# Kernel optimization log

Measured on AMD Instinct MI355X. Metric: run time of the kernel, lower is better.

Reference implementation:

```python
import jax, jax.numpy as jnp
import numpy as np

L, S, B, E, H, FF = 512, 2048, 4, 1024, 16, 2048
HD = E // H  # 64


def _layernorm(x, g, b, eps=1e-5):
    m = jnp.mean(x, axis=-1, keepdims=True)
    v = jnp.mean((x - m) ** 2, axis=-1, keepdims=True)
    return (x - m) * jax.lax.rsqrt(v + eps) * g + b


def _decoder(tgt, memory, pos, query_pos,
             in_proj_w, in_proj_b, out_w, out_b,
             cq_w, cq_b, ck_w, ck_b, cv_w, cv_b,
             down_w, down_b, lin1_w, lin1_b, lin2_w, lin2_b,
             n1_g, n1_b, n2_g, n2_b, n3_g, n3_b):
    Lq, Bb, Em = tgt.shape
    scale = 1.0 / np.sqrt(HD).astype(np.float32)
    # --- self attention (torch nn.MultiheadAttention, eval mode, no masks) ---
    qk_in = tgt + query_pos
    Wq, Wk, Wv = jnp.split(in_proj_w, 3, axis=0)
    bq, bk, bv = jnp.split(in_proj_b, 3)
    q = (qk_in @ Wq.T + bq).reshape(Lq, Bb, H, HD)
    k = (qk_in @ Wk.T + bk).reshape(Lq, Bb, H, HD)
    v = (tgt @ Wv.T + bv).reshape(Lq, Bb, H, HD)
    attn = jax.nn.softmax(jnp.einsum('lbhd,mbhd->bhlm', q, k) * scale, axis=-1)
    ctx = jnp.einsum('bhlm,mbhd->lbhd', attn, v).reshape(Lq, Bb, Em)
    tgt = _layernorm(tgt + ctx @ out_w.T + out_b, n1_g, n1_b)
    # --- custom cross attention; inputs permuted to [B, E, N] (Conv1d k=1 == matmul) ---
    qc = jnp.einsum('oe,lbe->bol', cq_w, tgt + query_pos) + cq_b[None, :, None]
    kc = jnp.einsum('oe,sbe->bos', ck_w, memory + pos) + ck_b[None, :, None]
    vc = jnp.einsum('oe,sbe->bos', cv_w, memory) + cv_b[None, :, None]
    # view(B, head_dim, num_heads, N): channel axis splits as (HD, H)
    qc = qc.reshape(Bb, HD, H, -1)
    kc = kc.reshape(Bb, HD, H, -1)
    vc = vc.reshape(Bb, HD, H, -1)
    # scores_2[b,d,h,m] = kc[b,d,h,m] * sum_{d',n} qc[b,d',h,n] kc[b,d',h,m] / sqrt(HD)
    # (einsum('abcd,aced->abcd', key, scores_1) broadcasts key over the summed n axis)
    s1sum = jnp.einsum('bdh,bdhm->bhm', qc.sum(-1), kc) * scale
    prob = jax.nn.softmax(kc * s1sum[:, None, :, :], axis=-1)        # [B,HD,H,S]
    o = jnp.einsum('bnhm,bdhm->bdhn', prob, vc)                       # [B,HD,H,HD]
    o = (o @ down_w.T + down_b).reshape(Bb, Em, 1)                    # Linear HD->1, then view
    tgt = _layernorm(tgt + jnp.transpose(o, (2, 0, 1)), n2_g, n2_b)   # [1,B,E] broadcasts over L
    # --- FFN ---
    ff = jax.nn.relu(tgt @ lin1_w.T + lin1_b) @ lin2_w.T + lin2_b
    return _layernorm(tgt + ff, n3_g, n3_b)


def setup_inputs() -> dict:
    key = jax.random.key(0)
    ks = jax.random.split(key, 16)
    def nrm(k, shape, s=0.02):
        return (s * jax.random.normal(k, shape)).astype(jnp.float32)
    z = lambda *s: jnp.zeros(s, jnp.float32)
    return dict(
        tgt=nrm(ks[0], (L, B, E), 1.0),
        memory=nrm(ks[1], (S, B, E), 1.0),
        pos=nrm(ks[2], (S, B, E), 1.0),
        query_pos=nrm(ks[3], (L, B, E), 1.0),
        in_proj_w=nrm(ks[4], (3 * E, E)), in_proj_b=z(3 * E),
        out_w=nrm(ks[5], (E, E)), out_b=z(E),
        cq_w=nrm(ks[6], (E, E)), cq_b=z(E),
        ck_w=nrm(ks[7], (E, E)), ck_b=z(E),
        cv_w=nrm(ks[8], (E, E)), cv_b=z(E),
        down_w=nrm(ks[9], (1, HD)), down_b=z(1),
        lin1_w=nrm(ks[10], (FF, E)), lin1_b=z(FF),
        lin2_w=nrm(ks[11], (E, FF)), lin2_b=z(E),
        n1_g=jnp.ones((E,), jnp.float32), n1_b=z(E),
        n2_g=jnp.ones((E,), jnp.float32), n2_b=z(E),
        n3_g=jnp.ones((E,), jnp.float32), n3_b=z(E),
    )


def reference(tgt, memory, pos, query_pos,
              in_proj_w, in_proj_b, out_w, out_b,
              cq_w, cq_b, ck_w, ck_b, cv_w, cv_b,
              down_w, down_b, lin1_w, lin1_b, lin2_w, lin2_b,
              n1_g, n1_b, n2_g, n2_b, n3_g, n3_b):
    return _decoder(tgt, memory, pos, query_pos,
                    in_proj_w, in_proj_b, out_w, out_b,
                    cq_w, cq_b, ck_w, ck_b, cv_w, cv_b,
                    down_w, down_b, lin1_w, lin1_b, lin2_w, lin2_b,
                    n1_g, n1_b, n2_g, n2_b, n3_g, n3_b)
```

## Files before the change

kernel.cpp:

```cpp
#include <hip/hip_runtime.h>
#include <hip/hip_bf16.h>

typedef __hip_bfloat16 bf16;
typedef short short8 __attribute__((ext_vector_type(8)));
typedef float f32x4 __attribute__((ext_vector_type(4)));

#define Lq 512
#define Sm 2048
#define Bb 4
#define Ee 1024
#define Hh 16
#define FFd 2048
#define HDd 64

static __device__ __forceinline__ float b2f(bf16 x) { return __bfloat162float(x); }
static __device__ __forceinline__ bf16 f2b(float x) { return __float2bfloat16(x); }
static __device__ __forceinline__ unsigned short bits(bf16 x) {
    return __builtin_bit_cast(unsigned short, x);
}
static __device__ __forceinline__ float us2f(unsigned short u) {
    return b2f(__builtin_bit_cast(bf16, u));
}

static __device__ __forceinline__ void gload16(const void* g, void* l) {
    __builtin_amdgcn_global_load_lds(
        (const __attribute__((address_space(1))) unsigned int*)g,
        (__attribute__((address_space(3))) unsigned int*)l, 16, 0, 0);
}

static __device__ __forceinline__ short8 pack8(float4 a0, float4 a1) {
    short8 u;
    u[0] = (short)bits(f2b(a0.x)); u[1] = (short)bits(f2b(a0.y));
    u[2] = (short)bits(f2b(a0.z)); u[3] = (short)bits(f2b(a0.w));
    u[4] = (short)bits(f2b(a1.x)); u[5] = (short)bits(f2b(a1.y));
    u[6] = (short)bits(f2b(a1.z)); u[7] = (short)bits(f2b(a1.w));
    return u;
}

__global__ __launch_bounds__(512, 2)
void kcvc_gemm(const bf16* __restrict__ wk, const bf16* __restrict__ wv,
               const bf16* __restrict__ mp, const bf16* __restrict__ mo,
               bf16* __restrict__ kc, bf16* __restrict__ vc,
               const float* __restrict__ kb, const float* __restrict__ vb)
{
    constexpr int BK = 64;
    __shared__ bf16 lA[2][256 * BK];
    __shared__ bf16 lB[2][256 * BK];

    const int tid  = threadIdx.x;
    const int lane = tid & 63;
    const int wm = (tid >> 6) >> 2;
    const int wn = (tid >> 6) & 3;

    int bid = (blockIdx.x & 7) * 32 + (blockIdx.x >> 3);
    const int bx = bid & 3;
    const int by = (bid >> 2) & 7;
    const int z  = bid >> 5;

    const bool isv = z >= 4;
    const int  b   = isv ? z - 4 : z;
    const bf16*  A    = isv ? wv : wk;
    const bf16*  B    = (isv ? mo : mp) + b * 1024;
    bf16*        C    = (isv ? vc : kc) + (long)b * 2097152;
    const float* bias = isv ? vb : kb;

    const int m0 = bx * 256, n0 = by * 256;
    const bf16* Abase = A + (long)m0 * 1024;
    const bf16* Bbase = B + (long)n0 * 4096;

    const int kgrp = lane >> 4, l16 = lane & 15;
    const int rsw = l16 & 7;

    auto stage = [&](int buf, int k0) {
#pragma unroll
        for (int r = 0; r < 4; r++) {
            int c = r * 512 + tid;
            int row = c >> 3;
            int ss = (c & 7) ^ (row & 7);
            gload16(Abase + (long)row * 1024 + k0 + ss * 8, &lA[buf][c * 8]);
        }
#pragma unroll
        for (int r = 0; r < 4; r++) {
            int c = r * 512 + tid;
            int row = c >> 3;
            int ss = (c & 7) ^ (row & 7);
            gload16(Bbase + (long)row * 4096 + k0 + ss * 8, &lB[buf][c * 8]);
        }
    };

    f32x4 acc[8][4];
#pragma unroll
    for (int i = 0; i < 8; i++)
#pragma unroll
        for (int j = 0; j < 4; j++) acc[i][j] = f32x4{0.f, 0.f, 0.f, 0.f};

    stage(0, 0);
    asm volatile("s_waitcnt vmcnt(0)" ::: "memory");
    __builtin_amdgcn_s_barrier();

    constexpr int NT = 16;
    for (int t = 0; t < NT; t++) {
        if (t + 1 < NT) stage((t + 1) & 1, (t + 1) * BK);

        const bf16* la = lA[t & 1];
        const bf16* lb = lB[t & 1];
#pragma unroll
        for (int h = 0; h < 2; h++) {
            const int sd = ((h * 4 + kgrp) ^ rsw) * 8;
            short8 af[8], bv[4];
#pragma unroll
            for (int i = 0; i < 8; i++)
                af[i] = *(const short8*)&la[(wm * 128 + i * 16 + l16) * BK + sd];
#pragma unroll
            for (int j = 0; j < 4; j++)
                bv[j] = *(const short8*)&lb[(wn * 64 + j * 16 + l16) * BK + sd];
            __builtin_amdgcn_s_setprio(1);
#pragma unroll
            for (int i = 0; i < 8; i++)
#pragma unroll
                for (int j = 0; j < 4; j++)
                    acc[i][j] = __builtin_amdgcn_mfma_f32_16x16x32_bf16(af[i], bv[j], acc[i][j], 0, 0, 0);
            __builtin_amdgcn_s_setprio(0);
        }

        asm volatile("s_waitcnt vmcnt(0)" ::: "memory");
        __builtin_amdgcn_s_barrier();
    }

#pragma unroll
    for (int i = 0; i < 8; i++) {
#pragma unroll
        for (int j = 0; j < 4; j++) {
#pragma unroll
            for (int r = 0; r < 4; r++) {
                int row = m0 + wm * 128 + i * 16 + kgrp * 4 + r;
                int col = n0 + wn * 64 + j * 16 + l16;
                float v = acc[i][j][r] + bias[row];
                float v2 = __shfl_xor(v, 1);
                if (!(l16 & 1)) {
                    unsigned int pk = (unsigned int)bits(f2b(v)) |
                                      ((unsigned int)bits(f2b(v2)) << 16);
                    *(unsigned int*)&C[(long)row * 2048 + col] = pk;
                }
            }
        }
    }
}

__global__ __launch_bounds__(512, 2)
void flash_attn(const bf16* __restrict__ qk, const bf16* __restrict__ vt,
                bf16* __restrict__ ctx)
{
    __shared__ bf16 lQ[128 * 64];
    __shared__ bf16 lK[2][64 * 64];
    __shared__ bf16 lV[2][64 * 64];
    __shared__ bf16 lP[128 * 64];
    __shared__ float scb[128];

    const int tid  = threadIdx.x;
    const int lane = tid & 63;
    const int wq   = tid >> 6;
    const int kgrp = lane >> 4, l16 = lane & 15;

    const int qt = blockIdx.x & 3;
    const int bh = blockIdx.x >> 2;
    const int b = bh >> 4, h = bh & 15;
    const int L0 = qt * 128;

#pragma unroll
    for (int it = 0; it < 2; it++) {
        int c = it * 512 + tid;
        int rr = c >> 3, sl = c & 7, ss = sl ^ (rr & 7);
        gload16(qk + ((long)(L0 + rr) * 4 + b) * 2048 + h * 64 + ss * 8,
                &lQ[(it * 512 + wq * 64) * 8]);
    }

    auto stageKV = [&](int buf, int st) {
        int rr = tid >> 3, sl = tid & 7, ss = sl ^ (rr & 7);
        gload16(qk + ((long)(st * 64 + rr) * 4 + b) * 2048 + 1024 + h * 64 + ss * 8,
                &lK[buf][(wq * 64) * 8]);
        gload16(vt + ((long)(b * 1024 + h * 64 + rr)) * 512 + st * 64 + ss * 8,
                &lV[buf][(wq * 64) * 8]);
    };

    auto frag = [&](const bf16* base, int row, int kk) {
        return *(const short8*)&base[row * 64 + (((kk * 4 + kgrp) ^ (l16 & 7)) * 8)];
    };

    f32x4 acc_o[4];
#pragma unroll
    for (int j = 0; j < 4; j++) acc_o[j] = f32x4{0.f, 0.f, 0.f, 0.f};
    float m_run = -1e30f, l_run = 0.f;

    stageKV(0, 0);
    asm volatile("s_waitcnt vmcnt(0)" ::: "memory");
    __builtin_amdgcn_s_barrier();

    int buf = 0;
    for (int st = 0; st < 8; st++) {
        if (st < 7) stageKV(buf ^ 1, st + 1);

        f32x4 accs[4];
#pragma unroll
        for (int fm = 0; fm < 4; fm++) accs[fm] = f32x4{0.f, 0.f, 0.f, 0.f};
        __builtin_amdgcn_s_setprio(1);
#pragma unroll
        for (int kk = 0; kk < 2; kk++) {
            short8 bq = frag(lQ, wq * 16 + l16, kk);
#pragma unroll
            for (int fm = 0; fm < 4; fm++) {
                short8 af = frag(lK[buf], fm * 16 + l16, kk);
                accs[fm] = __builtin_amdgcn_mfma_f32_16x16x32_bf16(af, bq, accs[fm], 0, 0, 0);
            }
        }
        __builtin_amdgcn_s_setprio(0);

        float v[4][4], p[4][4];
        float tmax = -1e30f;
#pragma unroll
        for (int fm = 0; fm < 4; fm++)
#pragma unroll
            for (int r = 0; r < 4; r++) {
                v[fm][r] = accs[fm][r] * 0.125f;
                tmax = fmaxf(tmax, v[fm][r]);
            }
        tmax = fmaxf(tmax, __shfl_xor(tmax, 16));
        tmax = fmaxf(tmax, __shfl_xor(tmax, 32));
        float m_new = fmaxf(m_run, tmax);
        float sc = __expf(m_run - m_new);
        float sum = 0.f;
#pragma unroll
        for (int fm = 0; fm < 4; fm++)
#pragma unroll
            for (int r = 0; r < 4; r++) {
                p[fm][r] = __expf(v[fm][r] - m_new);
                sum += p[fm][r];
            }
        sum += __shfl_xor(sum, 16);
        sum += __shfl_xor(sum, 32);
        l_run = l_run * sc + sum;
        m_run = m_new;

        if (!kgrp) scb[wq * 16 + l16] = sc;
        asm volatile("s_waitcnt lgkmcnt(0)" ::: "memory");
        __builtin_amdgcn_sched_barrier(0);
        float sc2[4];
#pragma unroll
        for (int r = 0; r < 4; r++) sc2[r] = scb[wq * 16 + kgrp * 4 + r];
#pragma unroll
        for (int fn = 0; fn < 4; fn++)
#pragma unroll
            for (int r = 0; r < 4; r++) acc_o[fn][r] *= sc2[r];

#pragma unroll
        for (int fm = 0; fm < 4; fm++) {
            int l = wq * 16 + l16;
            int sp = (fm * 2 + (kgrp >> 1)) ^ (l16 & 7);
            uint2 pk;
            pk.x = (unsigned int)bits(f2b(p[fm][0])) | ((unsigned int)bits(f2b(p[fm][1])) << 16);
            pk.y = (unsigned int)bits(f2b(p[fm][2])) | ((unsigned int)bits(f2b(p[fm][3])) << 16);
            *(uint2*)&lP[l * 64 + sp * 8 + (kgrp & 1) * 4] = pk;
        }
        asm volatile("s_waitcnt lgkmcnt(0)" ::: "memory");
        __builtin_amdgcn_sched_barrier(0);

        __builtin_amdgcn_s_setprio(1);
#pragma unroll
        for (int kk = 0; kk < 2; kk++) {
            short8 ap = frag(lP, wq * 16 + l16, kk);
#pragma unroll
            for (int fn = 0; fn < 4; fn++) {
                short8 bvf = frag(lV[buf], fn * 16 + l16, kk);
                acc_o[fn] = __builtin_amdgcn_mfma_f32_16x16x32_bf16(ap, bvf, acc_o[fn], 0, 0, 0);
            }
        }
        __builtin_amdgcn_s_setprio(0);

        asm volatile("s_waitcnt vmcnt(0)" ::: "memory");
        __builtin_amdgcn_s_barrier();
        buf ^= 1;
    }

    if (!kgrp) scb[wq * 16 + l16] = 1.f / l_run;
    asm volatile("s_waitcnt lgkmcnt(0)" ::: "memory");
    __builtin_amdgcn_sched_barrier(0);
    float inv[4];
#pragma unroll
    for (int r = 0; r < 4; r++) inv[r] = scb[wq * 16 + kgrp * 4 + r];
#pragma unroll
    for (int fn = 0; fn < 4; fn++) {
#pragma unroll
        for (int r = 0; r < 4; r++) {
            int lg = L0 + wq * 16 + kgrp * 4 + r;
            int d  = fn * 16 + l16;
            float vv = acc_o[fn][r] * inv[r];
            float v2 = __shfl_xor(vv, 1);
            if (!(l16 & 1)) {
                unsigned int pk = (unsigned int)bits(f2b(vv)) |
                                  ((unsigned int)bits(f2b(v2)) << 16);
                *(unsigned int*)&ctx[((long)lg * 4 + b) * 1024 + h * 64 + d] = pk;
            }
        }
    }
}

template<int BM, int BN>
__global__ __launch_bounds__(256)
void gemm_nt(const bf16* __restrict__ A, const bf16* __restrict__ Bw,
             float* __restrict__ Cf, bf16* __restrict__ Cb,
             const float* __restrict__ bias,
             const bf16* __restrict__ A2, const bf16* __restrict__ B2,
             bf16* __restrict__ Cb2, const float* __restrict__ bias2,
             int gx, int gy,
             int K, long lda, long ldb, long ldc,
             long sA1, long sA2, long sB1, long sB2, long sC1, long sC2,
             int zdiv, int zsplit, int nsplit, float alpha, int mode, int mode2)
{
    constexpr int BK = 64;
    constexpr int RA = BM / 32, RB = BN / 32;
    __shared__ bf16 lA[2][BM * BK];
    __shared__ bf16 lB[2][BN * BK];

    const int tid  = threadIdx.x;
    const int lane = tid & 63;
    const int wave = tid >> 6;
    const int wm = wave >> 1, wn = wave & 1;
    constexpr int RM = BM / 2, RN = BN / 2;
    constexpr int FM = RM / 16, FN = RN / 16;

    const int nwg = gridDim.x;
    const int cpx = nwg >> 3;
    int bid = (blockIdx.x & 7) * cpx + (blockIdx.x >> 3);
    const int bx = bid % gx;
    int tmp = bid / gx;
    const int by = tmp % gy;
    const int z  = tmp / gy;

    const int m0 = bx * BM;
    const int n0 = by * BN;

    const bool use2 = (z >= zsplit) || (n0 >= nsplit);
    const int  zz   = (z >= zsplit) ? z - zsplit : z;
    const bf16*  Ap = (use2 && A2)    ? A2    : A;
    const bf16*  Bp = (use2 && B2)    ? B2    : Bw;
    const float* bp = (use2 && bias2) ? bias2 : bias;
    const int    md = use2 ? mode2 : mode;
    bf16*        Co = (use2 && Cb2)   ? Cb2   : Cb;

    const long offA = (long)(zz / zdiv) * sA1 + (long)(zz % zdiv) * sA2;
    const long offB = (long)(zz / zdiv) * sB1 + (long)(zz % zdiv) * sB2;
    const long offC = (long)(zz / zdiv) * sC1 + (long)(zz % zdiv) * sC2;

    const bf16* Abase = Ap + offA + (long)m0 * lda;
    const bf16* Bbase = Bp + offB + (long)n0 * ldb;

    const int kgrp = lane >> 4;
    const int l16  = lane & 15;
    const int rsw  = l16 & 7;

    auto stage = [&](int buf, int k0) {
#pragma unroll
        for (int r = 0; r < RA; r++) {
            int c = r * 256 + tid;
            int row = c >> 3;
            int ss = (c & 7) ^ (row & 7);
            gload16(Abase + (long)row * lda + k0 + ss * 8, &lA[buf][c * 8]);
        }
#pragma unroll
        for (int r = 0; r < RB; r++) {
            int c = r * 256 + tid;
            int row = c >> 3;
            int ss = (c & 7) ^ (row & 7);
            gload16(Bbase + (long)row * ldb + k0 + ss * 8, &lB[buf][c * 8]);
        }
    };

    f32x4 acc[FM][FN];
#pragma unroll
    for (int i = 0; i < FM; i++)
#pragma unroll
        for (int j = 0; j < FN; j++) acc[i][j] = f32x4{0.f, 0.f, 0.f, 0.f};

    const int nt = K / BK;
    stage(0, 0);
    asm volatile("s_waitcnt vmcnt(0)" ::: "memory");
    __builtin_amdgcn_s_barrier();

    for (int t = 0; t < nt; t++) {
        if (t + 1 < nt) stage((t + 1) & 1, (t + 1) * BK);

        const bf16* la = lA[t & 1];
        const bf16* lb = lB[t & 1];
#pragma unroll
        for (int h = 0; h < 2; h++) {
            const int sd = ((h * 4 + kgrp) ^ rsw) * 8;
            short8 af[FM], bv[FN];
#pragma unroll
            for (int i = 0; i < FM; i++)
                af[i] = *(const short8*)&la[(wm * RM + i * 16 + l16) * BK + sd];
#pragma unroll
            for (int j = 0; j < FN; j++)
                bv[j] = *(const short8*)&lb[(wn * RN + j * 16 + l16) * BK + sd];
            __builtin_amdgcn_s_setprio(1);
#pragma unroll
            for (int i = 0; i < FM; i++)
#pragma unroll
                for (int j = 0; j < FN; j++)
                    acc[i][j] = __builtin_amdgcn_mfma_f32_16x16x32_bf16(af[i], bv[j], acc[i][j], 0, 0, 0);
            __builtin_amdgcn_s_setprio(0);
        }

        asm volatile("s_waitcnt vmcnt(0)" ::: "memory");
        __builtin_amdgcn_s_barrier();
    }

#pragma unroll
    for (int i = 0; i < FM; i++) {
#pragma unroll
        for (int j = 0; j < FN; j++) {
#pragma unroll
            for (int r = 0; r < 4; r++) {
                int row = m0 + wm * RM + i * 16 + kgrp * 4 + r;
                int col = n0 + wn * RN + j * 16 + l16;
                float v = alpha * acc[i][j][r] + (bp ? bp[col] : 0.f);
                float v2 = __shfl_xor(v, 1);
                if (md == 0) {
                    if (!(l16 & 1)) {
                        float2 pv = {v, v2};
                        *(float2*)&Cf[offC + (long)row * ldc + col] = pv;
                    }
                } else if (md == 1) {
                    if (!(l16 & 1)) {
                        unsigned int pk = (unsigned int)bits(f2b(v)) |
                                          ((unsigned int)bits(f2b(v2)) << 16);
                        *(unsigned int*)&Co[offC + (long)row * ldc + col] = pk;
                    }
                } else if (md == 2) {
                    if (!(l16 & 1)) {
                        unsigned int pk = (unsigned int)bits(f2b(fmaxf(v, 0.f))) |
                                          ((unsigned int)bits(f2b(fmaxf(v2, 0.f))) << 16);
                        *(unsigned int*)&Co[offC + (long)row * ldc + col] = pk;
                    }
                } else {
                    int o = col - nsplit;
                    Cb2[((long)(row & 3) * 1024 + o) * 512 + (row >> 2)] = f2b(v);
                }
            }
        }
    }
}

struct Cvt2Seg { const float* a; const float* b; bf16* d; bf16* d2; int nblk; };
struct Cvt2Args { Cvt2Seg s[8]; };

__global__ __launch_bounds__(256)
void cvt_kernel(Cvt2Args args)
{
    for (int ci = blockIdx.x; ci < 10240; ci += 2048) {
        int rem = ci;
        int si = 0;
        while (si < 7 && rem >= args.s[si].nblk) { rem -= args.s[si].nblk; si++; }
        Cvt2Seg sg = args.s[si];
        const long i = (long)rem * 2048 + threadIdx.x * 8;

        float4 a0 = *(const float4*)(sg.a + i);
        float4 a1 = *(const float4*)(sg.a + i + 4);
        float4 s0 = a0, s1 = a1;
        if (sg.b) {
            float4 b0 = *(const float4*)(sg.b + i);
            float4 b1 = *(const float4*)(sg.b + i + 4);
            s0.x += b0.x; s0.y += b0.y; s0.z += b0.z; s0.w += b0.w;
            s1.x += b1.x; s1.y += b1.y; s1.z += b1.z; s1.w += b1.w;
        }
        *(short8*)((unsigned short*)sg.d + i) = pack8(s0, s1);
        if (sg.d2) {
            *(short8*)((unsigned short*)sg.d2 + i) = pack8(a0, a1);
        }
    }
}

__global__ __launch_bounds__(256)
void ln_kernel(const float* __restrict__ x, const bf16* __restrict__ xB,
               const float* __restrict__ res, const float* __restrict__ resb,
               const float* __restrict__ g, const float* __restrict__ be,
               float* __restrict__ outF, bf16* __restrict__ outB)
{
    long row = blockIdx.x;
    int tid = threadIdx.x, lane = tid & 63, w = tid >> 6;
    float vv[4];
    if (x) {
        float4 xv = *(const float4*)(x + row * 1024 + tid * 4);
        vv[0] = xv.x; vv[1] = xv.y; vv[2] = xv.z; vv[3] = xv.w;
    } else {
        ushort4 xv = *(const ushort4*)((const unsigned short*)xB + row * 1024 + tid * 4);
        vv[0] = us2f(xv.x); vv[1] = us2f(xv.y); vv[2] = us2f(xv.z); vv[3] = us2f(xv.w);
    }
    if (res) {
        float4 rv = *(const float4*)(res + row * 1024 + tid * 4);
        vv[0] += rv.x; vv[1] += rv.y; vv[2] += rv.z; vv[3] += rv.w;
    }
    if (resb) {
        float4 rv = *(const float4*)(resb + (row & 3) * 1024 + tid * 4);
        vv[0] += rv.x; vv[1] += rv.y; vv[2] += rv.z; vv[3] += rv.w;
    }
    float s = vv[0] + vv[1] + vv[2] + vv[3];
    float q = vv[0] * vv[0] + vv[1] * vv[1] + vv[2] * vv[2] + vv[3] * vv[3];
    __shared__ float rs[4], rq[4];
    for (int o = 32; o; o >>= 1) { s += __shfl_xor(s, o); q += __shfl_xor(q, o); }
    if (!lane) { rs[w] = s; rq[w] = q; }
    __syncthreads();
    s = rs[0] + rs[1] + rs[2] + rs[3];
    q = rq[0] + rq[1] + rq[2] + rq[3];
    float mean = s * (1.f / 1024.f);
    float var  = q * (1.f / 1024.f) - mean * mean;
    float rstd = rsqrtf(var + 1e-5f);
    float4 gv = *(const float4*)(g + tid * 4);
    float4 bv = *(const float4*)(be + tid * 4);
    float o0 = (vv[0] - mean) * rstd * gv.x + bv.x;
    float o1 = (vv[1] - mean) * rstd * gv.y + bv.y;
    float o2 = (vv[2] - mean) * rstd * gv.z + bv.z;
    float o3 = (vv[3] - mean) * rstd * gv.w + bv.w;
    if (outF) {
        float4 ov = {o0, o1, o2, o3};
        *(float4*)(outF + row * 1024 + tid * 4) = ov;
    }
    if (outB) {
        ushort4 u;
        u.x = bits(f2b(o0)); u.y = bits(f2b(o1));
        u.z = bits(f2b(o2)); u.w = bits(f2b(o3));
        *reinterpret_cast<ushort4*>((unsigned short*)outB + row * 1024 + tid * 4) = u;
    }
}

__global__ __launch_bounds__(256)
void asum_part_kernel(const float* __restrict__ t1, const float* __restrict__ qp,
                      float* __restrict__ part)
{
    int blk = blockIdx.x;
    int lc = blk >> 4, b = (blk >> 2) & 3, ec = blk & 3;
    int e = ec * 256 + threadIdx.x;
    float acc = 0.f;
#pragma unroll 4
    for (int l = lc * 32; l < lc * 32 + 32; l++) {
        long idx = ((long)(l * 4 + b)) * 1024 + e;
        acc += t1[idx] + qp[idx];
    }
    part[(lc * 4 + b) * 1024 + e] = acc;
}

__global__ __launch_bounds__(256)
void asum_reduce_kernel(const float* __restrict__ part, float* __restrict__ asum)
{
    int b = blockIdx.x >> 2, ec = blockIdx.x & 3;
    int e = ec * 256 + threadIdx.x;
    float acc = 0.f;
#pragma unroll
    for (int lc = 0; lc < 16; lc++) acc += part[(lc * 4 + b) * 1024 + e];
    asum[b * 1024 + e] = acc;
}

__global__ __launch_bounds__(256)
void qsum_kernel(const float* __restrict__ cqw, const float* __restrict__ cqb,
                 const float* __restrict__ asum, float* __restrict__ qsum)
{
    int o = blockIdx.x * 4 + (threadIdx.x >> 6);
    int lane = threadIdx.x & 63;
    float a0 = 0, a1 = 0, a2 = 0, a3 = 0;
    for (int j = 0; j < 16; j++) {
        int e = lane + j * 64;
        float wv = cqw[(long)o * 1024 + e];
        a0 += wv * asum[e];
        a1 += wv * asum[1024 + e];
        a2 += wv * asum[2048 + e];
        a3 += wv * asum[3072 + e];
    }
    for (int t = 32; t; t >>= 1) {
        a0 += __shfl_xor(a0, t); a1 += __shfl_xor(a1, t);
        a2 += __shfl_xor(a2, t); a3 += __shfl_xor(a3, t);
    }
    if (!lane) {
        float bb = 512.f * cqb[o];
        qsum[o] = a0 + bb; qsum[1024 + o] = a1 + bb;
        qsum[2048 + o] = a2 + bb; qsum[3072 + o] = a3 + bb;
    }
}

__global__ __launch_bounds__(256)
void s1_kernel(const bf16* __restrict__ kc, const float* __restrict__ qsum,
               float* __restrict__ s1)
{
    int bh = blockIdx.x, b = bh >> 4, h = bh & 15;
    int m = blockIdx.y * 256 + threadIdx.x;
    __shared__ float qd[64];
    if (threadIdx.x < 64) qd[threadIdx.x] = qsum[b * 1024 + threadIdx.x * 16 + h];
    __syncthreads();
    const bf16* kcb = kc + (long)b * 2048 * 1024 + (long)h * 2048 + m;
    float acc = 0.f;
#pragma unroll 8
    for (int d = 0; d < 64; d++) acc += qd[d] * b2f(kcb[(long)d * 16 * 2048]);
    s1[(long)bh * 2048 + m] = acc * 0.125f;
}

__global__ __launch_bounds__(256)
void bsum_kernel(const bf16* __restrict__ kc, const float* __restrict__ s1,
                 float* __restrict__ rmax, float* __restrict__ rsum)
{
    int bh = blockIdx.x >> 6, n = blockIdx.x & 63;
    int b = bh >> 4, h = bh & 15;
    int tid = threadIdx.x, lane = tid & 63, w = tid >> 6;
    const bf16* row = kc + (long)b * 2048 * 1024 + (long)(n * 16 + h) * 2048;
    const float* s1r = s1 + (long)bh * 2048;
    float t[8];
    float mx = -1e30f;
#pragma unroll
    for (int i = 0; i < 8; i++) {
        int m = tid + i * 256;
        t[i] = b2f(row[m]) * s1r[m];
        mx = fmaxf(mx, t[i]);
    }
    __shared__ float redm[4], reds[4];
    for (int o = 32; o; o >>= 1) mx = fmaxf(mx, __shfl_xor(mx, o));
    if (!lane) redm[w] = mx;
    __syncthreads();
    mx = fmaxf(fmaxf(redm[0], redm[1]), fmaxf(redm[2], redm[3]));
    float s = 0.f;
#pragma unroll
    for (int i = 0; i < 8; i++) s += __expf(t[i] - mx);
    for (int o = 32; o; o >>= 1) s += __shfl_xor(s, o);
    if (!lane) reds[w] = s;
    __syncthreads();
    if (!tid) {
        rmax[bh * 64 + n] = mx;
        rsum[bh * 64 + n] = reds[0] + reds[1] + reds[2] + reds[3];
    }
}

__global__ __launch_bounds__(256)
void wpr_kernel(const bf16* __restrict__ kc, const float* __restrict__ s1,
                const float* __restrict__ rmax, const float* __restrict__ rsum,
                const float* __restrict__ dw, float* __restrict__ wpr)
{
    int bh = blockIdx.x, b = bh >> 4, h = bh & 15;
    int m = blockIdx.y * 256 + threadIdx.x;
    __shared__ float cf[64], cm[64];
    if (threadIdx.x < 64) {
        cf[threadIdx.x] = dw[threadIdx.x] / rsum[bh * 64 + threadIdx.x];
        cm[threadIdx.x] = rmax[bh * 64 + threadIdx.x];
    }
    __syncthreads();
    float s1v = s1[(long)bh * 2048 + m];
    const bf16* kcb = kc + (long)b * 2048 * 1024 + (long)h * 2048 + m;
    float acc = 0.f;
#pragma unroll 8
    for (int n = 0; n < 64; n++)
        acc += cf[n] * __expf(b2f(kcb[(long)n * 16 * 2048]) * s1v - cm[n]);
    wpr[(long)bh * 2048 + m] = acc;
}

__global__ __launch_bounds__(256)
void cout_kernel(const bf16* __restrict__ vc, const float* __restrict__ wpr,
                 const float* __restrict__ db, float* __restrict__ outs)
{
    int bh = blockIdx.x >> 2, dg = blockIdx.x & 3;
    int b = bh >> 4, h = bh & 15;
    int tid = threadIdx.x, lane = tid & 63, w = tid >> 6;
    __shared__ float lwpr[2048];
#pragma unroll
    for (int i = 0; i < 8; i++) lwpr[tid + i * 256] = wpr[(long)bh * 2048 + tid + i * 256];
    __syncthreads();
#pragma unroll
    for (int dd = 0; dd < 4; dd++) {
        int d = dg * 16 + w * 4 + dd;
        int o = d * 16 + h;
        const bf16* vrow = vc + (long)b * 2048 * 1024 + (long)o * 2048;
        float acc = 0.f;
#pragma unroll
        for (int j = 0; j < 4; j++) {
            int m = j * 512 + lane * 8;
            short8 vv = *(const short8*)&vrow[m];
#pragma unroll
            for (int k = 0; k < 8; k++) {
                bf16 bb = __builtin_bit_cast(bf16, (unsigned short)vv[k]);
                acc += lwpr[m + k] * b2f(bb);
            }
        }
        for (int t2 = 32; t2; t2 >>= 1) acc += __shfl_xor(acc, t2);
        if (!lane) outs[b * 1024 + o] = acc + db[0];
    }
}

extern "C" void kernel_launch(void* const* d_in, const int* in_sizes, int n_in,
                              void* d_out, int out_size, void* d_ws, size_t ws_size,
                              hipStream_t stream)
{
    const float* tgt  = (const float*)d_in[0];
    const float* mem  = (const float*)d_in[1];
    const float* pos  = (const float*)d_in[2];
    const float* qp   = (const float*)d_in[3];
    const float* ipw  = (const float*)d_in[4];
    const float* ipb  = (const float*)d_in[5];
    const float* outw = (const float*)d_in[6];
    const float* outb = (const float*)d_in[7];
    const float* cqw  = (const float*)d_in[8];
    const float* cqb  = (const float*)d_in[9];
    const float* ckw  = (const float*)d_in[10];
    const float* ckb  = (const float*)d_in[11];
    const float* cvw  = (const float*)d_in[12];
    const float* cvb  = (const float*)d_in[13];
    const float* dww  = (const float*)d_in[14];
    const float* dwb  = (const float*)d_in[15];
    const float* l1w  = (const float*)d_in[16];
    const float* l1b  = (const float*)d_in[17];
    const float* l2w  = (const float*)d_in[18];
    const float* l2b  = (const float*)d_in[19];
    const float* n1g  = (const float*)d_in[20];
    const float* n1b  = (const float*)d_in[21];
    const float* n2g  = (const float*)d_in[22];
    const float* n2b  = (const float*)d_in[23];
    const float* n3g  = (const float*)d_in[24];
    const float* n3b  = (const float*)d_in[25];

    char* ws = (char*)d_ws;
    auto MB = [](long x) { return x << 20; };
    bf16* w_ip    = (bf16*)(ws + MB(0));
    bf16* w_out   = (bf16*)(ws + MB(6));
    bf16* w_ck    = (bf16*)(ws + MB(8));
    bf16* w_cv    = (bf16*)(ws + MB(10));
    bf16* w_l1    = (bf16*)(ws + MB(12));
    bf16* w_l2    = (bf16*)(ws + MB(16));
    bf16* qkin    = (bf16*)(ws + MB(20));
    bf16* tgtb    = (bf16*)(ws + MB(24));
    bf16* memposb = (bf16*)(ws + MB(28));
    bf16* memb    = (bf16*)(ws + MB(44));
    bf16* qkbuf   = (bf16*)(ws + MB(60));
    bf16* vtb     = (bf16*)(ws + MB(68));
    bf16* kcb     = (bf16*)(ws + MB(72));
    bf16* ctxb    = (bf16*)(ws + MB(104));
    bf16* atmpb   = (bf16*)(ws + MB(108));
    float* s1buf  = (float*)(ws + MB(108));
    float* wprbuf = (float*)(ws + MB(109));
    float* rmax   = (float*)(ws + MB(110));
    float* rsum   = (float*)(ws + MB(110) + (64 << 10));
    float* part   = (float*)(ws + MB(111));
    float* tgt1   = (float*)(ws + MB(116));
    float* asum   = (float*)(ws + MB(124));
    float* qsum   = (float*)(ws + MB(125));
    bf16* vcb     = (bf16*)(ws + MB(126));
    float* outs   = (float*)(ws + MB(142));
    float* tgt2   = (float*)(ws + MB(143));
    bf16* tgt2b   = (bf16*)(ws + MB(151));
    bf16* ff1b    = (bf16*)(ws + MB(155));
    bf16* ff2b    = (bf16*)(ws + MB(163));

    const int BIGZ = 1000000, BIGN = 1 << 30;

    Cvt2Args ca{};
    ca.s[0] = {ipw,  nullptr, w_ip,    nullptr, 1536};
    ca.s[1] = {outw, nullptr, w_out,   nullptr, 512};
    ca.s[2] = {ckw,  nullptr, w_ck,    nullptr, 512};
    ca.s[3] = {cvw,  nullptr, w_cv,    nullptr, 512};
    ca.s[4] = {l1w,  nullptr, w_l1,    nullptr, 1024};
    ca.s[5] = {l2w,  nullptr, w_l2,    nullptr, 1024};
    ca.s[6] = {tgt,  qp,      qkin,    tgtb,    1024};
    ca.s[7] = {mem,  pos,     memposb, memb,    4096};
    cvt_kernel<<<dim3(2048, 1, 1), 256, 0, stream>>>(ca);

    gemm_nt<64, 128><<<dim3(768, 1, 1), 256, 0, stream>>>(
        qkin, w_ip, nullptr, qkbuf, ipb,
        tgtb, nullptr, vtb, nullptr,
        32, 24,
        1024, 1024, 1024, 2048,
        0, 0, 0, 0, 0, 0, 1, BIGZ, 2048, 1.f, 1, 3);

    flash_attn<<<dim3(256, 1, 1), 512, 0, stream>>>(qkbuf, vtb, ctxb);

    gemm_nt<64, 128><<<dim3(256, 1, 1), 256, 0, stream>>>(
        ctxb, w_out, nullptr, atmpb, outb,
        nullptr, nullptr, nullptr, nullptr,
        32, 8,
        1024, 1024, 1024, 1024,
        0, 0, 0, 0, 0, 0, 1, BIGZ, BIGN, 1.f, 1, 1);

    ln_kernel<<<dim3(2048, 1, 1), 256, 0, stream>>>(
        nullptr, atmpb, tgt, nullptr, n1g, n1b, tgt1, nullptr);

    asum_part_kernel<<<dim3(256, 1, 1), 256, 0, stream>>>(tgt1, qp, part);
    asum_reduce_kernel<<<dim3(16, 1, 1), 256, 0, stream>>>(part, asum);
    qsum_kernel<<<dim3(256, 1, 1), 256, 0, stream>>>(cqw, cqb, asum, qsum);

    kcvc_gemm<<<dim3(256, 1, 1), 512, 0, stream>>>(
        w_ck, w_cv, memposb, memb, kcb, vcb, ckb, cvb);

    s1_kernel<<<dim3(64, 8, 1), 256, 0, stream>>>(kcb, qsum, s1buf);
    bsum_kernel<<<dim3(4096, 1, 1), 256, 0, stream>>>(kcb, s1buf, rmax, rsum);
    wpr_kernel<<<dim3(64, 8, 1), 256, 0, stream>>>(kcb, s1buf, rmax, rsum, dww, wprbuf);
    cout_kernel<<<dim3(256, 1, 1), 256, 0, stream>>>(vcb, wprbuf, dwb, outs);

    ln_kernel<<<dim3(2048, 1, 1), 256, 0, stream>>>(
        tgt1, nullptr, nullptr, outs, n2g, n2b, tgt2, tgt2b);

    gemm_nt<64, 128><<<dim3(512, 1, 1), 256, 0, stream>>>(
        tgt2b, w_l1, nullptr, ff1b, l1b,
        nullptr, nullptr, nullptr, nullptr,
        32, 16,
        1024, 1024, 1024, 2048,
        0, 0, 0, 0, 0, 0, 1, BIGZ, BIGN, 1.f, 2, 2);

    gemm_nt<64, 128><<<dim3(256, 1, 1), 256, 0, stream>>>(
        ff1b, w_l2, nullptr, ff2b, l2b,
        nullptr, nullptr, nullptr, nullptr,
        32, 8,
        2048, 2048, 2048, 1024,
        0, 0, 0, 0, 0, 0, 1, BIGZ, BIGN, 1.f, 1, 1);

    ln_kernel<<<dim3(2048, 1, 1), 256, 0, stream>>>(
        nullptr, ff2b, tgt2, nullptr, n3g, n3b, (float*)d_out, nullptr);
}
```

Before: 258.8 us.

## Overlap weight/memory fp32-to-bf16 conversion with flash attention via extra blocks

Moves most of the fp32-to-bf16 conversion work (out, ck, cv, lin1, lin2 weights and memory+pos) out of the up-front conversion kernel into 512 extra blocks appended to the flash attention launch. The conversion kernel now handles only the in-proj weight and tgt+query_pos needed by the first GEMM. The intent is to shorten the serial prologue and let the bandwidth-bound conversion run alongside the compute-bound attention, which only launches 256 blocks. The trade-off is that conversion blocks compete with attention blocks for CUs and memory bandwidth, and they carry the same large shared-memory footprint as the attention blocks, which may limit occupancy.

After: 249.3 us. -3.7%, faster.

```diff
diff --git a/kernel.cpp b/kernel.cpp
--- a/kernel.cpp
+++ b/kernel.cpp
@@ -36,6 +36,9 @@
     u[6] = (short)bits(f2b(a1.z)); u[7] = (short)bits(f2b(a1.w));
     return u;
 }
+
+struct Cvt2Seg { const float* a; const float* b; bf16* d; bf16* d2; int nblk; };
+struct Cvt2Args { Cvt2Seg s[8]; };
 
 __global__ __launch_bounds__(512, 2)
 void kcvc_gemm(const bf16* __restrict__ wk, const bf16* __restrict__ wv,
@@ -148,14 +151,40 @@
 }
 
 __global__ __launch_bounds__(512, 2)
-void flash_attn(const bf16* __restrict__ qk, const bf16* __restrict__ vt,
-                bf16* __restrict__ ctx)
+void flash_cvt(const bf16* __restrict__ qk, const bf16* __restrict__ vt,
+               bf16* __restrict__ ctx, Cvt2Args args)
 {
     __shared__ bf16 lQ[128 * 64];
     __shared__ bf16 lK[2][64 * 64];
     __shared__ bf16 lV[2][64 * 64];
     __shared__ bf16 lP[128 * 64];
     __shared__ float scb[128];
+
+    if (blockIdx.x >= 256) {
+        const int cb = blockIdx.x - 256;
+        for (int ci = cb; ci < 3840; ci += 512) {
+            int rem = ci;
+            int si = 0;
+            while (si < 5 && rem >= args.s[si].nblk) { rem -= args.s[si].nblk; si++; }
+            Cvt2Seg sg = args.s[si];
+            const long i = (long)rem * 4096 + threadIdx.x * 8;
+
+            float4 a0 = *(const float4*)(sg.a + i);
+            float4 a1 = *(const float4*)(sg.a + i + 4);
+            float4 s0 = a0, s1 = a1;
+            if (sg.b) {
+                float4 b0 = *(const float4*)(sg.b + i);
+                float4 b1 = *(const float4*)(sg.b + i + 4);
+                s0.x += b0.x; s0.y += b0.y; s0.z += b0.z; s0.w += b0.w;
+                s1.x += b1.x; s1.y += b1.y; s1.z += b1.z; s1.w += b1.w;
+            }
+            *(short8*)((unsigned short*)sg.d + i) = pack8(s0, s1);
+            if (sg.d2) {
+                *(short8*)((unsigned short*)sg.d2 + i) = pack8(a0, a1);
+            }
+        }
+        return;
+    }
 
     const int tid  = threadIdx.x;
     const int lane = tid & 63;
@@ -450,13 +479,10 @@
     }
 }
 
-struct Cvt2Seg { const float* a; const float* b; bf16* d; bf16* d2; int nblk; };
-struct Cvt2Args { Cvt2Seg s[8]; };
-
 __global__ __launch_bounds__(256)
 void cvt_kernel(Cvt2Args args)
 {
-    for (int ci = blockIdx.x; ci < 10240; ci += 2048) {
+    for (int ci = blockIdx.x; ci < 2560; ci += 2048) {
         int rem = ci;
         int si = 0;
         while (si < 7 && rem >= args.s[si].nblk) { rem -= args.s[si].nblk; si++; }
@@ -756,13 +782,7 @@
 
     Cvt2Args ca{};
     ca.s[0] = {ipw,  nullptr, w_ip,    nullptr, 1536};
-    ca.s[1] = {outw, nullptr, w_out,   nullptr, 512};
-    ca.s[2] = {ckw,  nullptr, w_ck,    nullptr, 512};
-    ca.s[3] = {cvw,  nullptr, w_cv,    nullptr, 512};
-    ca.s[4] = {l1w,  nullptr, w_l1,    nullptr, 1024};
-    ca.s[5] = {l2w,  nullptr, w_l2,    nullptr, 1024};
-    ca.s[6] = {tgt,  qp,      qkin,    tgtb,    1024};
-    ca.s[7] = {mem,  pos,     memposb, memb,    4096};
+    ca.s[1] = {tgt,  qp,      qkin,    tgtb,    1024};
     cvt_kernel<<<dim3(2048, 1, 1), 256, 0, stream>>>(ca);
 
     gemm_nt<64, 128><<<dim3(768, 1, 1), 256, 0, stream>>>(
@@ -772,7 +792,14 @@
         1024, 1024, 1024, 2048,
         0, 0, 0, 0, 0, 0, 1, BIGZ, 2048, 1.f, 1, 3);
 
-    flash_attn<<<dim3(256, 1, 1), 512, 0, stream>>>(qkbuf, vtb, ctxb);
+    Cvt2Args cd{};
+    cd.s[0] = {outw, nullptr, w_out,   nullptr, 256};
+    cd.s[1] = {ckw,  nullptr, w_ck,    nullptr, 256};
+    cd.s[2] = {cvw,  nullptr, w_cv,    nullptr, 256};
+    cd.s[3] = {l1w,  nullptr, w_l1,    nullptr, 512};
+    cd.s[4] = {l2w,  nullptr, w_l2,    nullptr, 512};
+    cd.s[5] = {mem,  pos,     memposb, memb,    2048};
+    flash_cvt<<<dim3(768, 1, 1), 512, 0, stream>>>(qkbuf, vtb, ctxb, cd);
 
     gemm_nt<64, 128><<<dim3(256, 1, 1), 256, 0, stream>>>(
         ctxb, w_out, nullptr, atmpb, outb,
```
